# Kernel optimization log

Hardware: AMD Instinct MI355X
Metric: run time of the kernel (lower is better)

## Reference

```python
import jax, jax.numpy as jnp
import numpy as np

# Static geometry config (mirrors TerminalConfig): positions and ranges that
# define the 3D neighborhood connection table.
X_POS, Y_POS, Z_POS = 10, 10, 10
XY_RANGE, Z_RANGE, Z_OFFSET = 3, 4, 1
B, S, D = 8, 4096, 2048
TOP_K = 8


def _build_connections():
    # torch.cartesian_prod(x_idx, y_idx, z_idx) -> [T, 3]
    xs = jnp.arange(X_POS - XY_RANGE, X_POS + XY_RANGE + 1)
    ys = jnp.arange(Y_POS - XY_RANGE, Y_POS + XY_RANGE + 1)
    zs = jnp.arange(Z_POS - Z_OFFSET, Z_POS + Z_RANGE - Z_OFFSET + 1)
    gx, gy, gz = jnp.meshgrid(xs, ys, zs, indexing='ij')
    return jnp.stack([gx.ravel(), gy.ravel(), gz.ravel()], axis=-1).astype(jnp.int32)


def setup_inputs() -> dict:
    key = jax.random.key(0)
    k1, k2 = jax.random.split(key)
    conn = _build_connections()           # [245, 3]
    T = conn.shape[0]
    x = jax.random.normal(k1, (B, S, D), dtype=jnp.float32)
    W_router = jax.random.normal(k2, (D, T), dtype=jnp.float32) * (1.0 / np.sqrt(D))
    b_router = jnp.zeros((T,), dtype=jnp.float32)
    return {"x": x, "W_router": W_router, "b_router": b_router,
            "neuron_connections": conn, "top_k": TOP_K}


def reference(x, W_router, b_router, neuron_connections, top_k):
    # Router: token features -> logit per candidate connection. [B,S,T]
    logits = jnp.einsum('bsd,dt->bst', x, W_router) + b_router
    # Sampler: softmax probabilities, top-k selection. [B,S,k]
    probs = jax.nn.softmax(logits, axis=-1)
    top_probs, indices = jax.lax.top_k(probs, top_k)
    # Gather precomputed connection coordinates. [B,S,k,3]
    selected_neurons = neuron_connections[indices]
    return (x, top_probs, selected_neurons)
```

## Files before the change

kernel.cpp:

```cpp
#include <hip/hip_runtime.h>
#include <math.h>

#define D_DIM 2048
#define T_N   245
#define TOPK  8
#define BM    64
#define NCH   32

typedef __attribute__((ext_vector_type(8))) __bf16 bf16x8;
typedef __attribute__((ext_vector_type(4))) float  f32x4;

#define WS_LIST_OFF   256
#define WS_WTP_OFF    (256 * 1024)

#define P_C    32768
#define P_FCG  2048
#define P_KS   1024
#define P_HL   512

__device__ __forceinline__ unsigned short bf16_rne(float f) {
    unsigned u = __builtin_bit_cast(unsigned, f);
    u += 0x7FFFu + ((u >> 16) & 1u);
    return (unsigned short)(u >> 16);
}
__device__ __forceinline__ float bf16_to_f(unsigned short h) {
    return __builtin_bit_cast(float, (unsigned)h << 16);
}

__device__ __forceinline__ void gll16(const float* g, float* l) {
    __builtin_amdgcn_global_load_lds(
        (const __attribute__((address_space(1))) void*)g,
        (__attribute__((address_space(3))) void*)l, 16, 0, 0);
}

__device__ __forceinline__ void split8(const float4& A, const float4& B,
                                       bf16x8& h8, bf16x8& l8) {
    const float f[8] = {A.x, A.y, A.z, A.w, B.x, B.y, B.z, B.w};
    unsigned hu[4], lu[4];
#pragma unroll
    for (int p = 0; p < 4; ++p) {
        unsigned uh;
        asm("v_cvt_pk_bf16_f32 %0, %1, %2" : "=v"(uh) : "v"(f[2*p]), "v"(f[2*p+1]));
        const float h0 = __builtin_bit_cast(float, uh << 16);
        const float h1 = __builtin_bit_cast(float, uh & 0xffff0000u);
        const float l0 = f[2*p] - h0;
        const float l1 = f[2*p+1] - h1;
        unsigned ul;
        asm("v_cvt_pk_bf16_f32 %0, %1, %2" : "=v"(ul) : "v"(l0), "v"(l1));
        hu[p] = uh; lu[p] = ul;
    }
    uint4 vh = make_uint4(hu[0], hu[1], hu[2], hu[3]);
    uint4 vl = make_uint4(lu[0], lu[1], lu[2], lu[3]);
    h8 = __builtin_bit_cast(bf16x8, vh);
    l8 = __builtin_bit_cast(bf16x8, vl);
}

__global__ __launch_bounds__(256)
void prep_pack(const float* __restrict__ W,
               unsigned* __restrict__ cnt,
               unsigned short* __restrict__ wtp)
{
    if (blockIdx.x == 0 && blockIdx.y == 0 && threadIdx.x == 0) *cnt = 0u;

    const int c   = blockIdx.x;
    const int fcg = blockIdx.y;
    const int tid = threadIdx.x;
    const int ks   = tid >> 7;
    const int hl   = (tid >> 6) & 1;
    const int lane = tid & 63;

    const int row = fcg * 16 + (lane & 15);
    const int kb  = c * 64 + ks * 32 + (lane >> 4) * 8;

    unsigned short v[8];
#pragma unroll
    for (int j = 0; j < 8; ++j) {
        const float f = (row < T_N) ? W[(long)(kb + j) * T_N + row] : 0.0f;
        const unsigned short h = bf16_rne(f);
        v[j] = hl ? bf16_rne(f - bf16_to_f(h)) : h;
    }
    const long off = (long)c * P_C + (long)fcg * P_FCG + ks * P_KS
                     + hl * P_HL + lane * 8;
    *reinterpret_cast<uint4*>(wtp + off) = *reinterpret_cast<const uint4*>(v);
}

__global__ __launch_bounds__(512, 2)
void router_mfma(const float* __restrict__ x,
                 const unsigned short* __restrict__ wtp,
                 const float* __restrict__ br,
                 const int*   __restrict__ conn,
                 float* __restrict__ out_x,
                 float* __restrict__ out_p,
                 float* __restrict__ out_n,
                 unsigned* __restrict__ cnt,
                 unsigned* __restrict__ list)
{
    __shared__ float smem[8320];

    const int tid  = threadIdx.x;
    const int lane = tid & 63;
    const int wid  = tid >> 6;
    const int wr   = wid >> 2;
    const int wc   = wid & 3;
    const int m16  = lane & 15;
    const int kq   = lane >> 4;
    const long row0 = (long)blockIdx.x * BM;

    f32x4 acc[2][4];
#pragma unroll
    for (int fr = 0; fr < 2; ++fr)
#pragma unroll
        for (int fc = 0; fc < 4; ++fc)
            acc[fr][fc] = (f32x4){0.f, 0.f, 0.f, 0.f};

    auto stage = [&](int c, int bufW) {
#pragma unroll
        for (int q = 0; q < 2; ++q) {
            const int rbase = wid * 8 + q * 4;
            const int r     = rbase + (lane >> 4);
            const int u     = (lane & 15) ^ (r & 15);
            gll16(x + (row0 + r) * (long)D_DIM + c * 64 + u * 4,
                  &smem[bufW + rbase * 64]);
        }
    };

    stage(0, 0);
    __syncthreads();

    for (int c = 0; c < NCH; ++c) {
        const int k0   = c * 64;
        const int bufW = (c & 1) * 4096;

        uint4 bh[4][2], bl[4][2];
        {
            const unsigned short* pc = wtp + (long)c * P_C + (long)wc * 4 * P_FCG
                                       + lane * 8;
#pragma unroll
            for (int fc = 0; fc < 4; ++fc)
#pragma unroll
                for (int ks = 0; ks < 2; ++ks) {
                    const unsigned short* p = pc + fc * P_FCG + ks * P_KS;
                    bh[fc][ks] = *reinterpret_cast<const uint4*>(p);
                    bl[fc][ks] = *reinterpret_cast<const uint4*>(p + P_HL);
                }
        }

        if (c + 1 < NCH) stage(c + 1, ((c + 1) & 1) * 4096);

        {
            const int row = tid >> 4;
            const int u   = tid & 15;
#pragma unroll
            for (int rg = 0; rg < 2; ++rg) {
                const int r = rg * 32 + row;
                f32x4 v = *reinterpret_cast<const f32x4*>(
                    &smem[bufW + r * 64 + (u ^ (r & 15)) * 4]);
                __builtin_nontemporal_store(v, reinterpret_cast<f32x4*>(
                    out_x + (row0 + r) * (long)D_DIM + k0 + u * 4));
            }
        }

#pragma unroll
        for (int ks = 0; ks < 2; ++ks) {
            bf16x8 ah[2], al[2];
#pragma unroll
            for (int fr = 0; fr < 2; ++fr) {
                const int row = wr * 32 + fr * 16 + m16;
                const int u0  = ks * 8 + kq * 2;
                float4 r0 = *reinterpret_cast<const float4*>(
                    &smem[bufW + row * 64 + ((u0)     ^ m16) * 4]);
                float4 r1 = *reinterpret_cast<const float4*>(
                    &smem[bufW + row * 64 + ((u0 + 1) ^ m16) * 4]);
                split8(r0, r1, ah[fr], al[fr]);
            }
            __builtin_amdgcn_s_setprio(1);
#pragma unroll
            for (int fc = 0; fc < 4; ++fc) {
                const bf16x8 bhv = __builtin_bit_cast(bf16x8, bh[fc][ks]);
                const bf16x8 blv = __builtin_bit_cast(bf16x8, bl[fc][ks]);
#pragma unroll
                for (int fr = 0; fr < 2; ++fr) {
                    acc[fr][fc] = __builtin_amdgcn_mfma_f32_16x16x32_bf16(ah[fr], bhv, acc[fr][fc], 0, 0, 0);
                    acc[fr][fc] = __builtin_amdgcn_mfma_f32_16x16x32_bf16(al[fr], bhv, acc[fr][fc], 0, 0, 0);
                    acc[fr][fc] = __builtin_amdgcn_mfma_f32_16x16x32_bf16(ah[fr], blv, acc[fr][fc], 0, 0, 0);
                }
            }
            __builtin_amdgcn_s_setprio(0);
        }
        __syncthreads();
    }

#pragma unroll 1
    for (int h = 0; h < 2; ++h) {
        __syncthreads();
        if (wr == h) {
#pragma unroll
            for (int fr = 0; fr < 2; ++fr)
#pragma unroll
                for (int fc = 0; fc < 4; ++fc)
#pragma unroll
                    for (int r = 0; r < 4; ++r) {
                        const int rloc = fr * 16 + kq * 4 + r;
                        const int col  = wc * 64 + fc * 16 + m16;
                        float v = acc[fr][fc][r];
                        v = (col < T_N) ? v + br[col] : -1e30f;
                        smem[rloc * 260 + col] = v;
                    }
        }
        __syncthreads();

        const int rloc = tid >> 4;
        const int sub  = tid & 15;
        const long gr  = row0 + h * 32 + rloc;
        const float* base = &smem[rloc * 260];

        float vals[16];
#pragma unroll
        for (int t = 0; t < 16; ++t) vals[t] = base[sub + 16 * t];

        float m = -INFINITY;
#pragma unroll
        for (int t = 0; t < 16; ++t) m = fmaxf(m, vals[t]);
#pragma unroll
        for (int d = 8; d >= 1; d >>= 1) m = fmaxf(m, __shfl_xor(m, d, 16));

        float e[16]; float s = 0.f;
#pragma unroll
        for (int t = 0; t < 16; ++t) { e[t] = expf(vals[t] - m); s += e[t]; }
#pragma unroll
        for (int d = 8; d >= 1; d >>= 1) s += __shfl_xor(s, d, 16);
        const float inv = 1.0f / s;

        unsigned chosen = 0u;
        float prev = INFINITY;
        int flag = 0;
#pragma unroll 1
        for (int k = 0; k < TOPK + 1; ++k) {
            float bv = -1.f; int bt = 0;
#pragma unroll
            for (int t = 0; t < 16; ++t)
                if (!((chosen >> t) & 1u) && e[t] > bv) { bv = e[t]; bt = t; }
            int bcol = sub + 16 * bt;
#pragma unroll
            for (int d = 8; d >= 1; d >>= 1) {
                const float ov = __shfl_xor(bv, d, 16);
                const int   oc = __shfl_xor(bcol, d, 16);
                if (ov > bv || (ov == bv && oc < bcol)) { bv = ov; bcol = oc; }
            }
            if (bv >= prev * 0.9998f) flag = 1;
            prev = bv;
            if (k < TOPK) {
                if ((bcol & 15) == sub) chosen |= 1u << (bcol >> 4);
                if (sub == 0) {
                    out_p[gr * TOPK + k] = bv * inv;
                    const int* cp = conn + bcol * 3;
                    out_n[(gr * TOPK + k) * 3 + 0] = (float)cp[0];
                    out_n[(gr * TOPK + k) * 3 + 1] = (float)cp[1];
                    out_n[(gr * TOPK + k) * 3 + 2] = (float)cp[2];
                }
            }
        }
        if (sub == 0 && flag) {
            unsigned idx = atomicAdd(cnt, 1u);
            if (idx < 32768u) list[idx] = (unsigned)gr;
        }
    }
}

#define RB 4
__global__ __launch_bounds__(512)
void refine_fp64(const float* __restrict__ x,
                 const float* __restrict__ W,
                 const float* __restrict__ br,
                 const int*   __restrict__ conn,
                 float* __restrict__ out_p,
                 float* __restrict__ out_n,
                 const unsigned* __restrict__ cnt,
                 const unsigned* __restrict__ list)
{
    __shared__ float  sx[RB][D_DIM];
    __shared__ double spart[2][RB][256];
    __shared__ double slog[RB][256];

    const int tid  = threadIdx.x;
    const int col  = tid & 255;
    const int kh   = tid >> 8;
    const int colc = (col < T_N) ? col : (T_N - 1);
    const int lane = tid & 63;
    const int w    = tid >> 6;
    const unsigned count = min(*cnt, 32768u);

    for (unsigned g0 = (unsigned)blockIdx.x * RB; g0 < count;
         g0 += gridDim.x * RB) {
        const int nb = (int)min((unsigned)RB, count - g0);
        long toks[RB];
#pragma unroll
        for (int j = 0; j < RB; ++j) {
            const unsigned idx = (g0 + j < count) ? (g0 + j) : (count - 1);
            toks[j] = (long)list[idx];
            *reinterpret_cast<float4*>(&sx[j][tid * 4]) =
                *reinterpret_cast<const float4*>(x + toks[j] * D_DIM + tid * 4);
        }
        __syncthreads();

        const int kb = kh * 1024;
        double a0 = 0.0, a1 = 0.0, a2 = 0.0, a3 = 0.0;
        for (int k0 = 0; k0 < 1024; k0 += 16) {
            float wv[16];
#pragma unroll
            for (int i = 0; i < 16; ++i)
                wv[i] = W[(long)(kb + k0 + i) * T_N + colc];
#pragma unroll
            for (int i = 0; i < 16; i += 2) {
                const float2 x0 = *reinterpret_cast<const float2*>(&sx[0][kb + k0 + i]);
                const float2 x1 = *reinterpret_cast<const float2*>(&sx[1][kb + k0 + i]);
                const float2 x2 = *reinterpret_cast<const float2*>(&sx[2][kb + k0 + i]);
                const float2 x3 = *reinterpret_cast<const float2*>(&sx[3][kb + k0 + i]);
                const double w0 = (double)wv[i], w1 = (double)wv[i + 1];
                a0 += (double)x0.x * w0; a0 += (double)x0.y * w1;
                a1 += (double)x1.x * w0; a1 += (double)x1.y * w1;
                a2 += (double)x2.x * w0; a2 += (double)x2.y * w1;
                a3 += (double)x3.x * w0; a3 += (double)x3.y * w1;
            }
        }
        spart[kh][0][col] = a0;
        spart[kh][1][col] = a1;
        spart[kh][2][col] = a2;
        spart[kh][3][col] = a3;
        __syncthreads();

        if (tid < 256) {
#pragma unroll
            for (int j = 0; j < RB; ++j)
                slog[j][tid] = (tid < T_N)
                    ? spart[0][j][tid] + spart[1][j][tid] + (double)br[tid]
                    : -1.0e300;
        }
        __syncthreads();

        if (w < nb) {
            const long tok = toks[w];
            double v[4];
#pragma unroll
            for (int i = 0; i < 4; ++i) v[i] = slog[w][lane + 64 * i];
            double m = fmax(fmax(v[0], v[1]), fmax(v[2], v[3]));
#pragma unroll
            for (int off = 32; off >= 1; off >>= 1)
                m = fmax(m, __shfl_xor(m, off));
            double e[4]; double s = 0.0;
#pragma unroll
            for (int i = 0; i < 4; ++i) {
                e[i] = (v[i] > -1.0e299) ? exp(v[i] - m) : 0.0;
                s += e[i];
            }
#pragma unroll
            for (int off = 32; off >= 1; off >>= 1)
                s += __shfl_xor(s, off);
            const double invZ = 1.0 / s;

            int sel[TOPK];
#pragma unroll 1
            for (int k = 0; k < TOPK; ++k) {
                double bv = -1.0; int bi = 255;
#pragma unroll
                for (int i = 0; i < 4; ++i) {
                    const int t = lane + 64 * i;
                    bool used = false;
                    for (int q = 0; q < k; ++q) used |= (sel[q] == t);
                    if (!used && e[i] > bv) { bv = e[i]; bi = t; }
                }
#pragma unroll
                for (int off = 32; off >= 1; off >>= 1) {
                    const double ov = __shfl_xor(bv, off);
                    const int    oi = __shfl_xor(bi, off);
                    if (ov > bv || (ov == bv && oi < bi)) { bv = ov; bi = oi; }
                }
                sel[k] = bi;
                if (lane == 0) {
                    out_p[tok * TOPK + k] = (float)(bv * invZ);
                    const int* cp = conn + bi * 3;
                    out_n[(tok * TOPK + k) * 3 + 0] = (float)cp[0];
                    out_n[(tok * TOPK + k) * 3 + 1] = (float)cp[1];
                    out_n[(tok * TOPK + k) * 3 + 2] = (float)cp[2];
                }
            }
        }
        __syncthreads();
    }
}

extern "C" void kernel_launch(void* const* d_in, const int* in_sizes, int n_in,
                              void* d_out, int out_size, void* d_ws, size_t ws_size,
                              hipStream_t stream) {
    const float* x    = (const float*)d_in[0];
    const float* Wr   = (const float*)d_in[1];
    const float* br   = (const float*)d_in[2];
    const int*   conn = (const int*)d_in[3];

    float* out_x = (float*)d_out;
    float* out_p = out_x + (size_t)8 * 4096 * 2048;
    float* out_n = out_p + (size_t)8 * 4096 * 8;

    unsigned*       cnt  = (unsigned*)d_ws;
    unsigned*       list = (unsigned*)((char*)d_ws + WS_LIST_OFF);
    unsigned short* wtp  = (unsigned short*)((char*)d_ws + WS_WTP_OFF);

    hipLaunchKernelGGL(prep_pack, dim3(32, 16), dim3(256), 0, stream,
                       Wr, cnt, wtp);
    hipLaunchKernelGGL(router_mfma, dim3(32768 / BM), dim3(512), 0, stream,
                       x, wtp, br, conn, out_x, out_p, out_n, cnt, list);
    hipLaunchKernelGGL(refine_fp64, dim3(512), dim3(512), 0, stream,
                       x, Wr, br, conn, out_p, out_n, cnt, list);
}
```

Baseline: 319.2 us.

## Software-pipeline W high-half loads across chunks and relax barrier waitcnt

Loads the high bf16 half of the next chunk's weight fragments one iteration early, using ping-pong register buffers and a loop unrolled by two. It replaces the full __syncthreads with a partial vmcnt wait plus s_barrier, so the prefetches stay in flight across the barrier. It also raises launch_bounds min blocks from 2 to 4. The risk is register pressure: the occupancy hint squeezes the VGPR budget while the prefetch buffers add live registers, which could cause spills. The hand-written vmcnt(10) must also match the real number of outstanding loads, or the LDS staging is wrong.

Result: slower. 662.8 us (+107.6%).

```diff
diff --git a/kernel.cpp b/kernel.cpp
--- a/kernel.cpp
+++ b/kernel.cpp
@@ -84,7 +84,7 @@
     *reinterpret_cast<uint4*>(wtp + off) = *reinterpret_cast<const uint4*>(v);
 }
 
-__global__ __launch_bounds__(512, 2)
+__global__ __launch_bounds__(512, 4)
 void router_mfma(const float* __restrict__ x,
                  const unsigned short* __restrict__ wtp,
                  const float* __restrict__ br,
@@ -123,29 +123,34 @@
                   &smem[bufW + rbase * 64]);
         }
     };
+    auto loadB = [&](int c, int hl, uint4 (&dst)[4][2]) {
+        const unsigned short* pc = wtp + (long)c * P_C + (long)wc * 4 * P_FCG
+                                   + hl * P_HL + lane * 8;
+#pragma unroll
+        for (int fc = 0; fc < 4; ++fc)
+#pragma unroll
+            for (int ks = 0; ks < 2; ++ks)
+                dst[fc][ks] = *reinterpret_cast<const uint4*>(
+                    pc + fc * P_FCG + ks * P_KS);
+    };
+
+    uint4 bhA[4][2], bhB[4][2];
 
     stage(0, 0);
+    loadB(0, 0, bhA);
     __syncthreads();
 
-    for (int c = 0; c < NCH; ++c) {
+    auto body = [&](int c, uint4 (&BP)[4][2], uint4 (&BN)[4][2]) {
         const int k0   = c * 64;
         const int bufW = (c & 1) * 4096;
 
-        uint4 bh[4][2], bl[4][2];
-        {
-            const unsigned short* pc = wtp + (long)c * P_C + (long)wc * 4 * P_FCG
-                                       + lane * 8;
-#pragma unroll
-            for (int fc = 0; fc < 4; ++fc)
-#pragma unroll
-                for (int ks = 0; ks < 2; ++ks) {
-                    const unsigned short* p = pc + fc * P_FCG + ks * P_KS;
-                    bh[fc][ks] = *reinterpret_cast<const uint4*>(p);
-                    bl[fc][ks] = *reinterpret_cast<const uint4*>(p + P_HL);
-                }
-        }
+        uint4 bl[4][2];
+        loadB(c, 1, bl);
 
         if (c + 1 < NCH) stage(c + 1, ((c + 1) & 1) * 4096);
+        __builtin_amdgcn_sched_barrier(0);
+
+        if (c + 1 < NCH) loadB(c + 1, 0, BN);
 
         {
             const int row = tid >> 4;
@@ -176,7 +181,7 @@
             __builtin_amdgcn_s_setprio(1);
 #pragma unroll
             for (int fc = 0; fc < 4; ++fc) {
-                const bf16x8 bhv = __builtin_bit_cast(bf16x8, bh[fc][ks]);
+                const bf16x8 bhv = __builtin_bit_cast(bf16x8, BP[fc][ks]);
                 const bf16x8 blv = __builtin_bit_cast(bf16x8, bl[fc][ks]);
 #pragma unroll
                 for (int fr = 0; fr < 2; ++fr) {
@@ -187,7 +192,18 @@
             }
             __builtin_amdgcn_s_setprio(0);
         }
-        __syncthreads();
+
+        if (c + 1 < NCH) {
+            __builtin_amdgcn_sched_barrier(0);
+            asm volatile("s_waitcnt vmcnt(10)" ::: "memory");
+            __builtin_amdgcn_s_barrier();
+            __builtin_amdgcn_sched_barrier(0);
+        }
+    };
+
+    for (int c = 0; c < NCH; c += 2) {
+        body(c,     bhA, bhB);
+        body(c + 1, bhB, bhA);
     }
 
 #pragma unroll 1
```
